# Performance work log

Hardware: AMD Instinct MI355X
Metric: run time of the kernel (lower is better)

Reference implementation:

```python
import jax, jax.numpy as jnp
import numpy as np

B, N, M, DQ, DK, DV, H = 8, 1024, 1024, 512, 512, 512, 8
DH = DV // H           # per-head dim (dim_split)
DFF = 4 * DV           # FFN hidden dim
EPS = 1e-5


def _layernorm(x, g, b):
    mu = jnp.mean(x, axis=-1, keepdims=True)
    var = jnp.mean(jnp.square(x - mu), axis=-1, keepdims=True)
    return (x - mu) * jax.lax.rsqrt(var + EPS) * g + b


def setup_inputs() -> dict:
    key = jax.random.key(0)
    ks = jax.random.split(key, 20)
    s = 0.02
    return {
        "Q": jax.random.normal(ks[0], (B, N, DQ), jnp.float32),
        "K": jax.random.normal(ks[1], (B, M, DK), jnp.float32),
        "Wq": jax.random.normal(ks[2], (DV, DQ), jnp.float32) * s,
        "bq": jnp.zeros((DV,), jnp.float32),
        "Wk": jax.random.normal(ks[3], (DV, DK), jnp.float32) * s,
        "bk": jnp.zeros((DV,), jnp.float32),
        "Wv": jax.random.normal(ks[4], (DV, DK), jnp.float32) * s,
        "bv": jnp.zeros((DV,), jnp.float32),
        "W1": jax.random.normal(ks[5], (DFF, DV), jnp.float32) * s,
        "b1": jnp.zeros((DFF,), jnp.float32),
        "W2": jax.random.normal(ks[6], (DFF, DFF), jnp.float32) * s,
        "b2": jnp.zeros((DFF,), jnp.float32),
        "W3": jax.random.normal(ks[7], (DV, DFF), jnp.float32) * s,
        "b3": jnp.zeros((DV,), jnp.float32),
        "g0": jnp.ones((DV,), jnp.float32),
        "beta0": jnp.zeros((DV,), jnp.float32),
        "g1": jnp.ones((DV,), jnp.float32),
        "beta1": jnp.zeros((DV,), jnp.float32),
    }


def reference(Q, K, Wq, bq, Wk, bk, Wv, bv, W1, b1, W2, b2, W3, b3, g0, beta0, g1, beta1):
    # projections (torch Linear: x @ W.T + b)
    Qp = Q @ Wq.T + bq            # [B, N, DV]
    Kp = K @ Wk.T + bk            # [B, M, DV]
    Vp = K @ Wv.T + bv            # [B, M, DV]

    # split heads: [B, S, DV] -> [B, S, H, DH]
    Qh = Qp.reshape(B, N, H, DH)
    Kh = Kp.reshape(B, M, H, DH)
    Vh = Vp.reshape(B, M, H, DH)

    # scaled dot-product attention (scale = sqrt(head_dim))
    A = jnp.einsum("bnhd,bmhd->bhnm", Qh, Kh) / jnp.sqrt(jnp.float32(DH))
    A = jax.nn.softmax(A, axis=-1)
    O = jnp.einsum("bhnm,bmhd->bnhd", A, Vh).reshape(B, N, DV)

    # residual with projected Q, then LN
    O = _layernorm(O + Qp, g0, beta0)

    # FFN: Linear->ReLU->Linear->ReLU->Linear (num_hidden_layers=2)
    h = jax.nn.relu(O @ W1.T + b1)
    h = jax.nn.relu(h @ W2.T + b2)
    Off = h @ W3.T + b3

    return _layernorm(O + Off, g1, beta1)
```

## Files before the change

### kernel.cpp

```cpp
#include <hip/hip_runtime.h>


typedef __bf16 bf16_t;
typedef __bf16 bf16x8 __attribute__((ext_vector_type(8)));
typedef __bf16 bf16x4 __attribute__((ext_vector_type(4)));
typedef __bf16 bf16x2 __attribute__((ext_vector_type(2)));
typedef float  f32x4  __attribute__((ext_vector_type(4)));
typedef float  f32x16 __attribute__((ext_vector_type(16)));
typedef int    i32x4_t __attribute__((ext_vector_type(4)));
typedef int    i32x8_t __attribute__((ext_vector_type(8)));

__device__ __forceinline__ f32x4 mfma16(bf16x8 a, bf16x8 b, f32x4 c) {
  return __builtin_amdgcn_mfma_f32_16x16x32_bf16(a, b, c, 0, 0, 0);
}

__device__ __forceinline__ void gload_lds16(const void* g, void* l) {
  __builtin_amdgcn_global_load_lds((const __attribute__((address_space(1))) void*)g,
                                   (__attribute__((address_space(3))) void*)l,
                                   16, 0, 0);
}

__device__ __forceinline__ unsigned char to_fp8(float v) {
  return (unsigned char)(__builtin_amdgcn_cvt_pk_fp8_f32(v, v, 0, false) & 0xff);
}

__global__ __launch_bounds__(256) void cast_all(
    const float* __restrict__ Q, const float* __restrict__ K,
    const float* __restrict__ Wq, const float* __restrict__ Wk,
    const float* __restrict__ Wv, const float* __restrict__ W1,
    const float* __restrict__ W2, const float* __restrict__ W3,
    bf16_t* Qb, bf16_t* Kb, bf16_t* Wqb, bf16_t* Wkb, bf16_t* Wvb,
    bf16_t* W1b, unsigned char* W2q, bf16_t* W3b)
{
  long i = ((long)blockIdx.x * 256 + threadIdx.x) * 4;
  if (i >= 10223616L && i < 14417920L) {
    long o = i - 10223616L;
    float4 v = *(const float4*)(W2 + o);
    unsigned int lo = __builtin_amdgcn_cvt_pk_fp8_f32(v.x, v.y, 0, false);
    unsigned int hi = __builtin_amdgcn_cvt_pk_fp8_f32(v.z, v.w, 0, false);
    *(unsigned int*)(W2q + o) = (lo & 0xffffu) | (hi << 16);
    return;
  }
  const float* s; bf16_t* d; long o;
  if      (i <  4194304L) { s = Q;  d = Qb;  o = i;             }
  else if (i <  8388608L) { s = K;  d = Kb;  o = i - 4194304L;  }
  else if (i <  8650752L) { s = Wq; d = Wqb; o = i - 8388608L;  }
  else if (i <  8912896L) { s = Wk; d = Wkb; o = i - 8650752L;  }
  else if (i <  9175040L) { s = Wv; d = Wvb; o = i - 8912896L;  }
  else if (i < 10223616L) { s = W1; d = W1b; o = i - 9175040L;  }
  else                    { s = W3; d = W3b; o = i - 14417920L; }
  float4 v = *(const float4*)(s + o);
  bf16x4 w;
  w[0] = (bf16_t)v.x; w[1] = (bf16_t)v.y; w[2] = (bf16_t)v.z; w[3] = (bf16_t)v.w;
  *(bf16x4*)(d + o) = w;
}

template <int BM, bool RELU, bool VTEPI, bool DBUF>
__device__ __forceinline__ void gemm_core(
    const bf16_t* __restrict__ A, const bf16_t* __restrict__ W,
    const float* __restrict__ bias, float* __restrict__ Cf,
    bf16_t* __restrict__ Cb, unsigned char* __restrict__ C8,
    bf16_t* __restrict__ VTout,
    float bscale, int N, int K, int lda, int ldb, int bx, int by)
{
  static_assert(BM == 128, "gemm_core tuned for BM=128");
  constexpr int FI = 4;
  constexpr int FJ = 4;
  constexpr int CN = 64;
  constexpr int AISS = 4;
  constexpr int SM_AB = (BM + 128) * 64 * 2;
  constexpr int SM_TS = 128 * 132 * 2;
  constexpr int SM_ONE = (VTEPI && SM_TS > SM_AB) ? SM_TS : SM_AB;
  constexpr int SMEM = DBUF ? 2 * SM_AB : SM_ONE;

  __shared__ __align__(16) char smem[SMEM];

  const int tid  = threadIdx.x;
  const int wave = tid >> 6, lane = tid & 63;
  const int lq   = lane & 15, quad = lane >> 4;
  const int wm   = wave & 1;
  const int wn   = wave >> 1;
  const long row0 = (long)bx * BM;
  const long col0 = (long)by * 128;

  const int sr = tid >> 3;
  const int cg = (tid & 7) ^ (sr & 7);
  const bf16_t* ag = A + (row0 + sr) * (long)lda + cg * 8;
  const bf16_t* bg = W + (col0 + sr) * (long)ldb + cg * 8;
  const int asOff = wave * 1024;
  const int bsOff = BM * 128 + wave * 1024;
  const long arows32 = 32L * lda;
  const long brows32 = 32L * ldb;

  auto stage = [&](int k0, int bi) {
    char* base = smem + (DBUF ? bi * SM_AB : 0);
#pragma unroll
    for (int is = 0; is < AISS; is++)
      gload_lds16(ag + is * arows32 + k0, base + asOff + is * 4096);
#pragma unroll
    for (int is = 0; is < 4; is++)
      gload_lds16(bg + is * brows32 + k0, base + bsOff + is * 4096);
  };

  const int off0 = (quad ^ (lq & 7)) * 8;
  const int aO0 = ((wm * 64 + lq) * 64 + off0) * 2;
  const int aO1 = ((wm * 64 + lq) * 64 + (off0 ^ 32)) * 2;
  const int bO0 = BM * 128 + ((wn * CN + lq) * 64 + off0) * 2;
  const int bO1 = BM * 128 + ((wn * CN + lq) * 64 + (off0 ^ 32)) * 2;

  f32x4 acc[FI][FJ];
#pragma unroll
  for (int i = 0; i < FI; i++)
#pragma unroll
    for (int j = 0; j < FJ; j++) acc[i][j] = (f32x4){0.f, 0.f, 0.f, 0.f};

  const int nt = K >> 6;
  if constexpr (DBUF) stage(0, 0);
  for (int t = 0; t < nt; ++t) {
    const char* base;
    if constexpr (DBUF) {
      const int cur = t & 1;
      if (t < nt - 1) {
        stage((t + 1) * 64, cur ^ 1);
        asm volatile("s_waitcnt vmcnt(8)" ::: "memory");
      } else {
        asm volatile("s_waitcnt vmcnt(0)" ::: "memory");
      }
      __builtin_amdgcn_s_barrier();
      __builtin_amdgcn_sched_barrier(0);
      base = smem + cur * SM_AB;
    } else {
      __syncthreads();
      stage(t * 64, 0);
      __syncthreads();
      base = smem;
    }

    bf16x8 af[FI], bw[FJ];
#pragma unroll
    for (int i = 0; i < FI; i++) af[i] = *(const bf16x8*)(base + aO0 + i * 2048);
#pragma unroll
    for (int j = 0; j < FJ; j++) bw[j] = *(const bf16x8*)(base + bO0 + j * 2048);
#pragma unroll
    for (int i = 0; i < FI; i++)
#pragma unroll
      for (int j = 0; j < FJ; j++)
        acc[i][j] = mfma16(af[i], bw[j], acc[i][j]);
#pragma unroll
    for (int i = 0; i < FI; i++) af[i] = *(const bf16x8*)(base + aO1 + i * 2048);
#pragma unroll
    for (int j = 0; j < FJ; j++) bw[j] = *(const bf16x8*)(base + bO1 + j * 2048);
#pragma unroll
    for (int i = 0; i < FI; i++)
#pragma unroll
      for (int j = 0; j < FJ; j++)
        acc[i][j] = mfma16(af[i], bw[j], acc[i][j]);

    if constexpr (DBUF) {
      __builtin_amdgcn_sched_barrier(0);
      __builtin_amdgcn_s_barrier();
    }
  }

  float bc[FJ];
#pragma unroll
  for (int j = 0; j < FJ; j++)
    bc[j] = bias ? bias[col0 + wn * CN + j * 16 + lq] : 0.f;

  if (VTEPI && VTout) {
    bf16_t* Ts = (bf16_t*)smem;
    __syncthreads();
#pragma unroll
    for (int i = 0; i < FI; i++)
#pragma unroll
      for (int j = 0; j < FJ; j++) {
        bf16x4 pv;
#pragma unroll
        for (int r = 0; r < 4; r++) pv[r] = (bf16_t)(acc[i][j][r] + bc[j]);
        *(bf16x4*)(Ts + (wn * CN + j * 16 + lq) * 132 + wm * 64 + i * 16 + quad * 4) = pv;
      }
    __syncthreads();
    const int b  = bx >> 3;
    const int mb = (bx & 7) * 128;
    const int h0 = by * 2;
    const int dd = tid >> 4;
    const int mc = (tid & 15) * 8;
#pragma unroll
    for (int p = 0; p < 8; p++) {
      const int d = dd + p * 16;
      bf16x8 v = *(const bf16x8*)(Ts + d * 132 + mc);
      *(bf16x8*)(VTout + ((long)(b * 8 + h0 + (d >> 6))) * 65536
                 + (d & 63) * 1024 + mb + mc) = v;
    }
    return;
  }

  const long rb = row0 + wm * 64 + quad * 4;
  const long cb = col0 + wn * CN + lq;
#pragma unroll
  for (int i = 0; i < FI; i++)
#pragma unroll
    for (int j = 0; j < FJ; j++)
#pragma unroll
      for (int r = 0; r < 4; r++) {
        float v = acc[i][j][r] + bc[j];
        if (RELU) v = fmaxf(v, 0.f);
        long idx = (rb + i * 16 + r) * (long)N + cb + j * 16;
        if (Cf) Cf[idx] = v;
        if (Cb) Cb[idx] = (bf16_t)(v * bscale);
        if (C8) C8[idx] = to_fp8(v);
      }
}

template <int BM, bool RELU>
__global__ __launch_bounds__(256) void gemm_bt(
    const bf16_t* __restrict__ A, const bf16_t* __restrict__ W,
    const float* __restrict__ bias, float* __restrict__ Cf,
    bf16_t* __restrict__ Cb, unsigned char* __restrict__ C8,
    float bscale, int N, int K)
{
  const int d  = blockIdx.x;
  const int bx = (d & 7) * 8 + ((d >> 3) & 7);
  const int by = d >> 6;
  gemm_core<BM, RELU, false, true>(A, W, bias, Cf, Cb, C8, nullptr, bscale,
                                   N, K, K, K, bx, by);
}

__global__ __launch_bounds__(256) void ffn3_splitk(
    const bf16_t* __restrict__ H2, const bf16_t* __restrict__ W3b,
    bf16_t* __restrict__ Off01)
{
  const int z = blockIdx.z;
  gemm_core<128, false, false, false>(H2 + z * 1024, W3b + z * 1024, nullptr,
                               nullptr, Off01 + (long)z * 4194304, nullptr,
                               nullptr, 1.0f, 512, 1024, 2048, 2048,
                               blockIdx.x, blockIdx.y);
}

__global__ __launch_bounds__(256) void proj3(
    const bf16_t* __restrict__ Qb, const bf16_t* __restrict__ Kb,
    const bf16_t* __restrict__ Wqb, const bf16_t* __restrict__ Wkb,
    const bf16_t* __restrict__ Wvb,
    const float* __restrict__ bq, const float* __restrict__ bk,
    const float* __restrict__ bv,
    bf16_t* Qpb, bf16_t* Kpb, bf16_t* VT)
{
  const int z = blockIdx.z;
  const bf16_t* A  = (z == 0) ? Qb : Kb;
  const bf16_t* Wt = (z == 0) ? Wqb : ((z == 1) ? Wkb : Wvb);
  const float* bias = (z == 0) ? bq : ((z == 1) ? bk : bv);
  bf16_t* Cb = (z == 0) ? Qpb : ((z == 1) ? Kpb : nullptr);
  bf16_t* VTout = (z == 2) ? VT : nullptr;
  const float sc = (z == 1) ? 0.125f : 1.0f;
  gemm_core<128, false, true, false>(A, Wt, bias, nullptr, Cb, nullptr, VTout, sc,
                              512, 512, 512, 512, blockIdx.x, blockIdx.y);
}

__global__ __launch_bounds__(256) void ffn2_fp8(
    const unsigned char* __restrict__ H1, const unsigned char* __restrict__ W2,
    const float* __restrict__ bias, bf16_t* __restrict__ C)
{
  __shared__ unsigned char As[16384];
  __shared__ unsigned char Bs[16384];
  const int tid = threadIdx.x;
  const int wave = tid >> 6, lane = tid & 63;
  const int wm = wave & 1, wn = wave >> 1;
  const int m = lane & 31, h = lane >> 5;
  const int d  = blockIdx.x;
  const int bxi = (d & 7) * 8 + ((d >> 3) & 7);
  const int byi = d >> 6;
  const long row0 = (long)bxi * 128;
  const long col0 = (long)byi * 128;

  const int sr = tid >> 3;
  const int cg = (tid & 7) ^ (sr & 7);
  const unsigned char* ag = H1 + (row0 + sr) * 2048 + cg * 16;
  const unsigned char* bg = W2 + (col0 + sr) * 2048 + cg * 16;
  char* asD = (char*)As + wave * 1024;
  char* bsD = (char*)Bs + wave * 1024;

  const int ar0 = wm * 64 + m, ar1 = ar0 + 32;
  const int br0 = wn * 64 + m, br1 = wn * 64 + 32 + m;

  f32x16 acc[2][2];
#pragma unroll
  for (int mi = 0; mi < 2; mi++)
#pragma unroll
    for (int nj = 0; nj < 2; nj++)
#pragma unroll
      for (int r = 0; r < 16; r++) acc[mi][nj][r] = 0.f;

  for (int k0 = 0; k0 < 2048; k0 += 128) {
    __syncthreads();
#pragma unroll
    for (int is = 0; is < 4; is++)
      gload_lds16(ag + is * 65536 + k0, asD + is * 4096);
#pragma unroll
    for (int is = 0; is < 4; is++)
      gload_lds16(bg + is * 65536 + k0, bsD + is * 4096);
    __syncthreads();
#pragma unroll
    for (int ks = 0; ks < 2; ks++) {
      const int c0 = ks * 4 + h * 2;
      i32x8_t a[2], b[2];
#pragma unroll
      for (int mi = 0; mi < 2; mi++) {
        const int r = mi ? ar1 : ar0;
        i32x4_t lo = *(const i32x4_t*)(As + r * 128 + ((c0    ) ^ (r & 7)) * 16);
        i32x4_t hi = *(const i32x4_t*)(As + r * 128 + ((c0 + 1) ^ (r & 7)) * 16);
        a[mi][0] = lo[0]; a[mi][1] = lo[1]; a[mi][2] = lo[2]; a[mi][3] = lo[3];
        a[mi][4] = hi[0]; a[mi][5] = hi[1]; a[mi][6] = hi[2]; a[mi][7] = hi[3];
      }
#pragma unroll
      for (int nj = 0; nj < 2; nj++) {
        const int r = nj ? br1 : br0;
        i32x4_t lo = *(const i32x4_t*)(Bs + r * 128 + ((c0    ) ^ (r & 7)) * 16);
        i32x4_t hi = *(const i32x4_t*)(Bs + r * 128 + ((c0 + 1) ^ (r & 7)) * 16);
        b[nj][0] = lo[0]; b[nj][1] = lo[1]; b[nj][2] = lo[2]; b[nj][3] = lo[3];
        b[nj][4] = hi[0]; b[nj][5] = hi[1]; b[nj][6] = hi[2]; b[nj][7] = hi[3];
      }
#pragma unroll
      for (int mi = 0; mi < 2; mi++)
#pragma unroll
        for (int nj = 0; nj < 2; nj++)
          acc[mi][nj] = __builtin_amdgcn_mfma_scale_f32_32x32x64_f8f6f4(
              a[mi], b[nj], acc[mi][nj], 0, 0,
              0, 0x7f7f7f7f, 0, 0x7f7f7f7f);
    }
  }

  float bc[2];
  bc[0] = bias[col0 + wn * 64 + m];
  bc[1] = bias[col0 + wn * 64 + 32 + m];
#pragma unroll
  for (int mi = 0; mi < 2; mi++)
#pragma unroll
    for (int nj = 0; nj < 2; nj++)
#pragma unroll
      for (int reg = 0; reg < 16; reg++) {
        const int rl = (reg & 3) + 8 * (reg >> 2) + 4 * h;
        float v = fmaxf(acc[mi][nj][reg] + bc[nj], 0.f);
        C[(row0 + wm * 64 + mi * 32 + rl) * 2048 + col0 + wn * 64 + nj * 32 + m]
            = (bf16_t)v;
      }
}

__global__ __launch_bounds__(256) void attn(
    const bf16_t* __restrict__ Qp, const bf16_t* __restrict__ Kp,
    const bf16_t* __restrict__ VT, bf16_t* __restrict__ O)
{
  const int d0 = blockIdx.x;
  const int j  = d0 >> 3;
  const int g  = (d0 & 7) * 8 + (j >> 3);
  const int qb = j & 7;
  const int h  = g & 7, b = g >> 3;

  const int tid = threadIdx.x;
  const int wave = tid >> 6, lane = tid & 63;
  const int lq = lane & 15, quad = lane >> 4;

  __shared__ bf16_t Ks[2][8192];
  __shared__ bf16_t VTs[2][8192];
  __shared__ bf16_t Ps[4][16 * 72];

  const long bh = (long)b * 1024;
  const int qrowA = qb * 128 + wave * 16 + lq;
  const int qrowB = qrowA + 64;

  const bf16_t* qpA = Qp + (bh + qrowA) * 512 + h * 64 + quad * 8;
  const bf16_t* qpB = Qp + (bh + qrowB) * 512 + h * 64 + quad * 8;
  const bf16x8 qfA0 = *(const bf16x8*)qpA;
  const bf16x8 qfA1 = *(const bf16x8*)(qpA + 32);
  const bf16x8 qfB0 = *(const bf16x8*)qpB;
  const bf16x8 qfB1 = *(const bf16x8*)(qpB + 32);

  f32x4 oaccA[4], oaccB[4];
#pragma unroll
  for (int t = 0; t < 4; t++) {
    oaccA[t] = (f32x4){0.f, 0.f, 0.f, 0.f};
    oaccB[t] = (f32x4){0.f, 0.f, 0.f, 0.f};
  }
  float lA = 0.f, lB = 0.f;

  const int sr = tid >> 3;
  const int cg = (tid & 7) ^ (sr & 7);
  const bf16_t* kg  = Kp + bh * 512 + h * 64;
  const bf16_t* vtg = VT + ((long)b * 8 + h) * 65536;
  const int off0 = (quad ^ (lq & 7)) * 8;

  auto stage = [&](int m0, int bi) {
    char* ksDst = (char*)(Ks[bi]) + wave * 1024;
    char* vtDst = (char*)(VTs[bi]) + wave * 1024;
#pragma unroll
    for (int s = 0; s < 2; s++) {
      gload_lds16(kg + (long)(m0 + s * 64 + sr) * 512 + cg * 8,      ksDst + s * 8192);
      gload_lds16(kg + (long)(m0 + s * 64 + sr + 32) * 512 + cg * 8, ksDst + s * 8192 + 4096);
      gload_lds16(vtg + (long)sr * 1024 + m0 + s * 64 + cg * 8,        vtDst + s * 8192);
      gload_lds16(vtg + (long)(sr + 32) * 1024 + m0 + s * 64 + cg * 8, vtDst + s * 8192 + 4096);
    }
  };

  stage(0, 0);

  for (int t = 0; t < 8; ++t) {
    const int cur = t & 1;
    if (t < 7) {
      stage((t + 1) * 128, cur ^ 1);
      asm volatile("s_waitcnt vmcnt(8)" ::: "memory");
    } else {
      asm volatile("s_waitcnt vmcnt(0)" ::: "memory");
    }
    __builtin_amdgcn_s_barrier();
    __builtin_amdgcn_sched_barrier(0);

    const bf16_t* Kc = Ks[cur];
    const bf16_t* Vc = VTs[cur];

    f32x4 stA[8], stB[8];
#pragma unroll
    for (int tt = 0; tt < 8; tt++) {
      const bf16_t* kb = Kc + (tt >> 2) * 4096 + ((tt & 3) * 16 + lq) * 64;
      bf16x8 ka0 = *(const bf16x8*)(kb + off0);
      bf16x8 ka1 = *(const bf16x8*)(kb + (off0 ^ 32));
      f32x4 sA = (f32x4){0.f, 0.f, 0.f, 0.f};
      sA = mfma16(ka0, qfA0, sA);
      sA = mfma16(ka1, qfA1, sA);
      stA[tt] = sA;
      f32x4 sB = (f32x4){0.f, 0.f, 0.f, 0.f};
      sB = mfma16(ka0, qfB0, sB);
      sB = mfma16(ka1, qfB1, sB);
      stB[tt] = sB;
    }

    float lsA = 0.f, lsB = 0.f;
#pragma unroll
    for (int tt = 0; tt < 8; tt++)
#pragma unroll
      for (int r = 0; r < 4; r++) {
        float pA = __expf(stA[tt][r]);
        stA[tt][r] = pA;
        lsA += pA;
        float pB = __expf(stB[tt][r]);
        stB[tt][r] = pB;
        lsB += pB;
      }
    lsA += __shfl_xor(lsA, 16, 64);
    lsA += __shfl_xor(lsA, 32, 64);
    lA += lsA;
    lsB += __shfl_xor(lsB, 16, 64);
    lsB += __shfl_xor(lsB, 32, 64);
    lB += lsB;

    bf16_t* pw = &Ps[wave][0];
#pragma unroll
    for (int hh = 0; hh < 2; hh++) {
#pragma unroll
      for (int tt = 0; tt < 4; tt++) {
        bf16x4 pv;
#pragma unroll
        for (int r = 0; r < 4; r++) pv[r] = (bf16_t)stA[hh * 4 + tt][r];
        *(bf16x4*)(pw + lq * 72 + tt * 16 + quad * 4) = pv;
      }
#pragma unroll
      for (int ks = 0; ks < 2; ks++) {
        bf16x8 pb = *(const bf16x8*)(pw + lq * 72 + ks * 32 + quad * 8);
#pragma unroll
        for (int dt = 0; dt < 4; dt++) {
          const bf16_t* vb = Vc + hh * 4096 + (dt * 16 + lq) * 64;
          bf16x8 va = *(const bf16x8*)(vb + (ks ? (off0 ^ 32) : off0));
          oaccA[dt] = mfma16(va, pb, oaccA[dt]);
        }
      }
    }
#pragma unroll
    for (int hh = 0; hh < 2; hh++) {
#pragma unroll
      for (int tt = 0; tt < 4; tt++) {
        bf16x4 pv;
#pragma unroll
        for (int r = 0; r < 4; r++) pv[r] = (bf16_t)stB[hh * 4 + tt][r];
        *(bf16x4*)(pw + lq * 72 + tt * 16 + quad * 4) = pv;
      }
#pragma unroll
      for (int ks = 0; ks < 2; ks++) {
        bf16x8 pb = *(const bf16x8*)(pw + lq * 72 + ks * 32 + quad * 8);
#pragma unroll
        for (int dt = 0; dt < 4; dt++) {
          const bf16_t* vb = Vc + hh * 4096 + (dt * 16 + lq) * 64;
          bf16x8 va = *(const bf16x8*)(vb + (ks ? (off0 ^ 32) : off0));
          oaccB[dt] = mfma16(va, pb, oaccB[dt]);
        }
      }
    }

    __builtin_amdgcn_sched_barrier(0);
    __builtin_amdgcn_s_barrier();
  }

  const float invA = 1.f / lA;
  const float invB = 1.f / lB;
  bf16_t* opA = O + (bh + qrowA) * 512 + h * 64 + quad * 4;
  bf16_t* opB = O + (bh + qrowB) * 512 + h * 64 + quad * 4;
#pragma unroll
  for (int dt = 0; dt < 4; dt++) {
    bf16x4 vA, vB;
#pragma unroll
    for (int r = 0; r < 4; r++) {
      vA[r] = (bf16_t)(oaccA[dt][r] * invA);
      vB[r] = (bf16_t)(oaccB[dt][r] * invB);
    }
    *(bf16x4*)(opA + dt * 16) = vA;
    *(bf16x4*)(opB + dt * 16) = vB;
  }
}

__device__ __forceinline__ float2 ld2(const float* p, long row, int tid) {
  return ((const float2*)(p + row * 512))[tid];
}
__device__ __forceinline__ float2 ld2(const bf16_t* p, long row, int tid) {
  bf16x2 v = *(const bf16x2*)(p + row * 512 + tid * 2);
  return make_float2((float)v[0], (float)v[1]);
}

__device__ __forceinline__ void ln_finish(
    float x0, float x1, const float* g, const float* be, int tid,
    int wave, int lane, float* of, bf16_t* ob, long row)
{
  float s = x0 + x1, ss = x0 * x0 + x1 * x1;
#pragma unroll
  for (int off = 1; off < 64; off <<= 1) {
    s  += __shfl_xor(s,  off, 64);
    ss += __shfl_xor(ss, off, 64);
  }
  __shared__ float sm[8];
  if (lane == 0) { sm[wave] = s; sm[4 + wave] = ss; }
  __syncthreads();
  s  = sm[0] + sm[1] + sm[2] + sm[3];
  ss = sm[4] + sm[5] + sm[6] + sm[7];
  const float mu = s * (1.f / 512.f);
  const float var = ss * (1.f / 512.f) - mu * mu;
  const float rs = rsqrtf(var + 1e-5f);
  const float2 gg = ((const float2*)g)[tid];
  const float2 bb = ((const float2*)be)[tid];
  const float o0 = (x0 - mu) * rs * gg.x + bb.x;
  const float o1 = (x1 - mu) * rs * gg.y + bb.y;
  if (of) ((float2*)(of + row * 512))[tid] = make_float2(o0, o1);
  if (ob) {
    bf16x2 t; t[0] = (bf16_t)o0; t[1] = (bf16_t)o1;
    *(bf16x2*)(ob + row * 512 + tid * 2) = t;
  }
}

__global__ __launch_bounds__(256) void ln_res(
    const bf16_t* __restrict__ A, const bf16_t* __restrict__ Bv,
    const float* __restrict__ g, const float* __restrict__ be,
    bf16_t* __restrict__ ob)
{
  const int row = blockIdx.x, tid = threadIdx.x;
  const float2 va = ld2(A,  (long)row, tid);
  const float2 vb = ld2(Bv, (long)row, tid);
  ln_finish(va.x + vb.x, va.y + vb.y, g, be, tid, tid >> 6, tid & 63,
            nullptr, ob, row);
}

__global__ __launch_bounds__(256) void ln_res3(
    const bf16_t* __restrict__ X, const bf16_t* __restrict__ O0,
    const bf16_t* __restrict__ O1, const float* __restrict__ bias,
    const float* __restrict__ g, const float* __restrict__ be,
    float* __restrict__ of)
{
  const int row = blockIdx.x, tid = threadIdx.x;
  const float2 vx = ld2(X,  (long)row, tid);
  const float2 v0 = ld2(O0, (long)row, tid);
  const float2 v1 = ld2(O1, (long)row, tid);
  const float2 vb = ((const float2*)bias)[tid];
  ln_finish(vx.x + v0.x + v1.x + vb.x, vx.y + v0.y + v1.y + vb.y,
            g, be, tid, tid >> 6, tid & 63, of, nullptr, row);
}

extern "C" void kernel_launch(void* const* d_in, const int* in_sizes, int n_in,
                              void* d_out, int out_size, void* d_ws, size_t ws_size,
                              hipStream_t stream)
{
  const float* Q   = (const float*)d_in[0];
  const float* K   = (const float*)d_in[1];
  const float* Wq  = (const float*)d_in[2];
  const float* bq  = (const float*)d_in[3];
  const float* Wk  = (const float*)d_in[4];
  const float* bk  = (const float*)d_in[5];
  const float* Wv  = (const float*)d_in[6];
  const float* bv  = (const float*)d_in[7];
  const float* W1  = (const float*)d_in[8];
  const float* b1  = (const float*)d_in[9];
  const float* W2  = (const float*)d_in[10];
  const float* b2  = (const float*)d_in[11];
  const float* W3  = (const float*)d_in[12];
  const float* b3  = (const float*)d_in[13];
  const float* g0  = (const float*)d_in[14];
  const float* be0 = (const float*)d_in[15];
  const float* g1  = (const float*)d_in[16];
  const float* be1 = (const float*)d_in[17];

  char* ws = (char*)d_ws;
  bf16_t* Wqb = (bf16_t*)(ws + 0);
  bf16_t* Wkb = (bf16_t*)(ws + 524288);
  bf16_t* Wvb = (bf16_t*)(ws + 1048576);
  bf16_t* W1b = (bf16_t*)(ws + 1572864);
  bf16_t* W3b = (bf16_t*)(ws + 3670016);
  unsigned char* W2q = (unsigned char*)(ws + 5767168);
  bf16_t* Qb  = (bf16_t*)(ws + 14155776);
  bf16_t* Kb  = (bf16_t*)(ws + 22544384);
  bf16_t* Qpb = (bf16_t*)(ws + 30932992);
  bf16_t* Kpb = (bf16_t*)(ws + 39321600);
  bf16_t* VT  = (bf16_t*)(ws + 47710208);
  bf16_t* Of  = (bf16_t*)(ws + 14155776);
  bf16_t* Xb  = (bf16_t*)(ws + 22544384);
  bf16_t* H2  = (bf16_t*)(ws + 30932992);
  unsigned char* H1q = (unsigned char*)(ws + 64487424);
  bf16_t* Off0 = (bf16_t*)(ws + 64487424);
  bf16_t* Off1 = (bf16_t*)(ws + 72876032);
  float*  out = (float*)d_out;

  cast_all<<<15104, 256, 0, stream>>>(Q, K, Wq, Wk, Wv, W1, W2, W3,
                                      Qb, Kb, Wqb, Wkb, Wvb, W1b, W2q, W3b);
  proj3<<<dim3(64, 4, 3), 256, 0, stream>>>(Qb, Kb, Wqb, Wkb, Wvb, bq, bk, bv,
                                            Qpb, Kpb, VT);
  attn<<<dim3(512, 1, 1), 256, 0, stream>>>(Qpb, Kpb, VT, Of);
  ln_res<<<8192, 256, 0, stream>>>(Of, Qpb, g0, be0, Xb);
  gemm_bt<128, true ><<<dim3(1024, 1, 1), 256, 0, stream>>>(Xb, W1b, b1, nullptr, nullptr, H1q, 1.0f, 2048, 512);
  ffn2_fp8<<<dim3(1024, 1, 1), 256, 0, stream>>>(H1q, W2q, b2, H2);
  ffn3_splitk<<<dim3(64, 4, 2), 256, 0, stream>>>(H2, W3b, Off0);
  ln_res3<<<8192, 256, 0, stream>>>(Xb, Off0, Off1, b3, g1, be1, out);
}
```

Measured before the change: 274.6 us.

## Move all FFN GEMMs to FP8 with a shared fp8 GEMM core

Quantizes W1 and W3 to FP8 alongside W2, has the first layernorm also emit an FP8 copy of its output, and runs FFN1, FFN2 and FFN3 through one templated FP8 MFMA GEMM core. FFN2 now writes FP8 activations instead of bf16, and FFN3 becomes an FP8 split-K GEMM. The goal is to halve operand bytes and use the faster FP8 MFMA path for the FFN. The cost is lower precision, which adds more error. The bf16 GEMM path drops double buffering since only proj3 still uses it, and the FFN launches lose the swizzled block ordering.

```diff
diff --git a/kernel.cpp b/kernel.cpp
--- a/kernel.cpp
+++ b/kernel.cpp
@@ -30,15 +30,18 @@
     const float* __restrict__ Wv, const float* __restrict__ W1,
     const float* __restrict__ W2, const float* __restrict__ W3,
     bf16_t* Qb, bf16_t* Kb, bf16_t* Wqb, bf16_t* Wkb, bf16_t* Wvb,
-    bf16_t* W1b, unsigned char* W2q, bf16_t* W3b)
+    unsigned char* W1q, unsigned char* W2q, unsigned char* W3q)
 {
   long i = ((long)blockIdx.x * 256 + threadIdx.x) * 4;
-  if (i >= 10223616L && i < 14417920L) {
-    long o = i - 10223616L;
-    float4 v = *(const float4*)(W2 + o);
+  if (i >= 9175040L) {
+    const float* s; unsigned char* d; long o;
+    if      (i < 10223616L) { s = W1; d = W1q; o = i - 9175040L;  }
+    else if (i < 14417920L) { s = W2; d = W2q; o = i - 10223616L; }
+    else                    { s = W3; d = W3q; o = i - 14417920L; }
+    float4 v = *(const float4*)(s + o);
     unsigned int lo = __builtin_amdgcn_cvt_pk_fp8_f32(v.x, v.y, 0, false);
     unsigned int hi = __builtin_amdgcn_cvt_pk_fp8_f32(v.z, v.w, 0, false);
-    *(unsigned int*)(W2q + o) = (lo & 0xffffu) | (hi << 16);
+    *(unsigned int*)(d + o) = (lo & 0xffffu) | (hi << 16);
     return;
   }
   const float* s; bf16_t* d; long o;
@@ -46,32 +49,26 @@
   else if (i <  8388608L) { s = K;  d = Kb;  o = i - 4194304L;  }
   else if (i <  8650752L) { s = Wq; d = Wqb; o = i - 8388608L;  }
   else if (i <  8912896L) { s = Wk; d = Wkb; o = i - 8650752L;  }
-  else if (i <  9175040L) { s = Wv; d = Wvb; o = i - 8912896L;  }
-  else if (i < 10223616L) { s = W1; d = W1b; o = i - 9175040L;  }
-  else                    { s = W3; d = W3b; o = i - 14417920L; }
+  else                    { s = Wv; d = Wvb; o = i - 8912896L;  }
   float4 v = *(const float4*)(s + o);
   bf16x4 w;
   w[0] = (bf16_t)v.x; w[1] = (bf16_t)v.y; w[2] = (bf16_t)v.z; w[3] = (bf16_t)v.w;
   *(bf16x4*)(d + o) = w;
 }
 
-template <int BM, bool RELU, bool VTEPI, bool DBUF>
+template <bool VTEPI>
 __device__ __forceinline__ void gemm_core(
     const bf16_t* __restrict__ A, const bf16_t* __restrict__ W,
-    const float* __restrict__ bias, float* __restrict__ Cf,
-    bf16_t* __restrict__ Cb, unsigned char* __restrict__ C8,
-    bf16_t* __restrict__ VTout,
+    const float* __restrict__ bias,
+    bf16_t* __restrict__ Cb, bf16_t* __restrict__ VTout,
     float bscale, int N, int K, int lda, int ldb, int bx, int by)
 {
-  static_assert(BM == 128, "gemm_core tuned for BM=128");
   constexpr int FI = 4;
   constexpr int FJ = 4;
   constexpr int CN = 64;
-  constexpr int AISS = 4;
-  constexpr int SM_AB = (BM + 128) * 64 * 2;
+  constexpr int SM_AB = 256 * 64 * 2;
   constexpr int SM_TS = 128 * 132 * 2;
-  constexpr int SM_ONE = (VTEPI && SM_TS > SM_AB) ? SM_TS : SM_AB;
-  constexpr int SMEM = DBUF ? 2 * SM_AB : SM_ONE;
+  constexpr int SMEM = (VTEPI && SM_TS > SM_AB) ? SM_TS : SM_AB;
 
   __shared__ __align__(16) char smem[SMEM];
 
@@ -80,7 +77,7 @@
   const int lq   = lane & 15, quad = lane >> 4;
   const int wm   = wave & 1;
   const int wn   = wave >> 1;
-  const long row0 = (long)bx * BM;
+  const long row0 = (long)bx * 128;
   const long col0 = (long)by * 128;
 
   const int sr = tid >> 3;
@@ -88,25 +85,24 @@
   const bf16_t* ag = A + (row0 + sr) * (long)lda + cg * 8;
   const bf16_t* bg = W + (col0 + sr) * (long)ldb + cg * 8;
   const int asOff = wave * 1024;
-  const int bsOff = BM * 128 + wave * 1024;
+  const int bsOff = 128 * 128 + wave * 1024;
   const long arows32 = 32L * lda;
   const long brows32 = 32L * ldb;
 
-  auto stage = [&](int k0, int bi) {
-    char* base = smem + (DBUF ? bi * SM_AB : 0);
-#pragma unroll
-    for (int is = 0; is < AISS; is++)
-      gload_lds16(ag + is * arows32 + k0, base + asOff + is * 4096);
+  auto stage = [&](int k0) {
 #pragma unroll
     for (int is = 0; is < 4; is++)
-      gload_lds16(bg + is * brows32 + k0, base + bsOff + is * 4096);
+      gload_lds16(ag + is * arows32 + k0, smem + asOff + is * 4096);
+#pragma unroll
+    for (int is = 0; is < 4; is++)
+      gload_lds16(bg + is * brows32 + k0, smem + bsOff + is * 4096);
   };
 
   const int off0 = (quad ^ (lq & 7)) * 8;
   const int aO0 = ((wm * 64 + lq) * 64 + off0) * 2;
   const int aO1 = ((wm * 64 + lq) * 64 + (off0 ^ 32)) * 2;
-  const int bO0 = BM * 128 + ((wn * CN + lq) * 64 + off0) * 2;
-  const int bO1 = BM * 128 + ((wn * CN + lq) * 64 + (off0 ^ 32)) * 2;
+  const int bO0 = 128 * 128 + ((wn * CN + lq) * 64 + off0) * 2;
+  const int bO1 = 128 * 128 + ((wn * CN + lq) * 64 + (off0 ^ 32)) * 2;
 
   f32x4 acc[FI][FJ];
 #pragma unroll
@@ -115,51 +111,30 @@
     for (int j = 0; j < FJ; j++) acc[i][j] = (f32x4){0.f, 0.f, 0.f, 0.f};
 
   const int nt = K >> 6;
-  if constexpr (DBUF) stage(0, 0);
   for (int t = 0; t < nt; ++t) {
-    const char* base;
-    if constexpr (DBUF) {
-      const int cur = t & 1;
-      if (t < nt - 1) {
-        stage((t + 1) * 64, cur ^ 1);
-        asm volatile("s_waitcnt vmcnt(8)" ::: "memory");
-      } else {
-        asm volatile("s_waitcnt vmcnt(0)" ::: "memory");
-      }
-      __builtin_amdgcn_s_barrier();
-      __builtin_amdgcn_sched_barrier(0);
-      base = smem + cur * SM_AB;
-    } else {
-      __syncthreads();
-      stage(t * 64, 0);
-      __syncthreads();
-      base = smem;
-    }
+    __syncthreads();
+    stage(t * 64);
+    __syncthreads();
 
     bf16x8 af[FI], bw[FJ];
 #pragma unroll
-    for (int i = 0; i < FI; i++) af[i] = *(const bf16x8*)(base + aO0 + i * 2048);
-#pragma unroll
-    for (int j = 0; j < FJ; j++) bw[j] = *(const bf16x8*)(base + bO0 + j * 2048);
+    for (int i = 0; i < FI; i++) af[i] = *(const bf16x8*)(smem + aO0 + i * 2048);
+#pragma unroll
+    for (int j = 0; j < FJ; j++) bw[j] = *(const bf16x8*)(smem + bO0 + j * 2048);
 #pragma unroll
     for (int i = 0; i < FI; i++)
 #pragma unroll
       for (int j = 0; j < FJ; j++)
         acc[i][j] = mfma16(af[i], bw[j], acc[i][j]);
 #pragma unroll
-    for (int i = 0; i < FI; i++) af[i] = *(const bf16x8*)(base + aO1 + i * 2048);
-#pragma unroll
-    for (int j = 0; j < FJ; j++) bw[j] = *(const bf16x8*)(base + bO1 + j * 2048);
+    for (int i = 0; i < FI; i++) af[i] = *(const bf16x8*)(smem + aO1 + i * 2048);
+#pragma unroll
+    for (int j = 0; j < FJ; j++) bw[j] = *(const bf16x8*)(smem + bO1 + j * 2048);
 #pragma unroll
     for (int i = 0; i < FI; i++)
 #pragma unroll
       for (int j = 0; j < FJ; j++)
         acc[i][j] = mfma16(af[i], bw[j], acc[i][j]);
-
-    if constexpr (DBUF) {
-      __builtin_amdgcn_sched_barrier(0);
-      __builtin_amdgcn_s_barrier();
-    }
   }
 
   float bc[FJ];
@@ -204,37 +179,9 @@
 #pragma unroll
       for (int r = 0; r < 4; r++) {
         float v = acc[i][j][r] + bc[j];
-        if (RELU) v = fmaxf(v, 0.f);
         long idx = (rb + i * 16 + r) * (long)N + cb + j * 16;
-        if (Cf) Cf[idx] = v;
         if (Cb) Cb[idx] = (bf16_t)(v * bscale);
-        if (C8) C8[idx] = to_fp8(v);
-      }
-}
-
-template <int BM, bool RELU>
-__global__ __launch_bounds__(256) void gemm_bt(
-    const bf16_t* __restrict__ A, const bf16_t* __restrict__ W,
-    const float* __restrict__ bias, float* __restrict__ Cf,
-    bf16_t* __restrict__ Cb, unsigned char* __restrict__ C8,
-    float bscale, int N, int K)
-{
-  const int d  = blockIdx.x;
-  const int bx = (d & 7) * 8 + ((d >> 3) & 7);
-  const int by = d >> 6;
-  gemm_core<BM, RELU, false, true>(A, W, bias, Cf, Cb, C8, nullptr, bscale,
-                                   N, K, K, K, bx, by);
-}
-
-__global__ __launch_bounds__(256) void ffn3_splitk(
-    const bf16_t* __restrict__ H2, const bf16_t* __restrict__ W3b,
-    bf16_t* __restrict__ Off01)
-{
-  const int z = blockIdx.z;
-  gemm_core<128, false, false, false>(H2 + z * 1024, W3b + z * 1024, nullptr,
-                               nullptr, Off01 + (long)z * 4194304, nullptr,
-                               nullptr, 1.0f, 512, 1024, 2048, 2048,
-                               blockIdx.x, blockIdx.y);
+      }
 }
 
 __global__ __launch_bounds__(256) void proj3(
@@ -252,13 +199,16 @@
   bf16_t* Cb = (z == 0) ? Qpb : ((z == 1) ? Kpb : nullptr);
   bf16_t* VTout = (z == 2) ? VT : nullptr;
   const float sc = (z == 1) ? 0.125f : 1.0f;
-  gemm_core<128, false, true, false>(A, Wt, bias, nullptr, Cb, nullptr, VTout, sc,
-                              512, 512, 512, 512, blockIdx.x, blockIdx.y);
-}
-
-__global__ __launch_bounds__(256) void ffn2_fp8(
-    const unsigned char* __restrict__ H1, const unsigned char* __restrict__ W2,
-    const float* __restrict__ bias, bf16_t* __restrict__ C)
+  gemm_core<true>(A, Wt, bias, Cb, VTout, sc,
+                  512, 512, 512, 512, blockIdx.x, blockIdx.y);
+}
+
+template <int OUT>
+__device__ __forceinline__ void fp8_gemm_core(
+    const unsigned char* __restrict__ A, const unsigned char* __restrict__ B,
+    const float* __restrict__ bias, unsigned char* __restrict__ C8,
+    bf16_t* __restrict__ Cb, int ldab, int K, int koff, int N,
+    int bxi, int byi)
 {
   __shared__ unsigned char As[16384];
   __shared__ unsigned char Bs[16384];
@@ -266,18 +216,16 @@
   const int wave = tid >> 6, lane = tid & 63;
   const int wm = wave & 1, wn = wave >> 1;
   const int m = lane & 31, h = lane >> 5;
-  const int d  = blockIdx.x;
-  const int bxi = (d & 7) * 8 + ((d >> 3) & 7);
-  const int byi = d >> 6;
   const long row0 = (long)bxi * 128;
   const long col0 = (long)byi * 128;
 
   const int sr = tid >> 3;
   const int cg = (tid & 7) ^ (sr & 7);
-  const unsigned char* ag = H1 + (row0 + sr) * 2048 + cg * 16;
-  const unsigned char* bg = W2 + (col0 + sr) * 2048 + cg * 16;
+  const unsigned char* ag = A + (row0 + sr) * (long)ldab + koff + cg * 16;
+  const unsigned char* bg = B + (col0 + sr) * (long)ldab + koff + cg * 16;
   char* asD = (char*)As + wave * 1024;
   char* bsD = (char*)Bs + wave * 1024;
+  const long rows32 = 32L * ldab;
 
   const int ar0 = wm * 64 + m, ar1 = ar0 + 32;
   const int br0 = wn * 64 + m, br1 = wn * 64 + 32 + m;
@@ -290,14 +238,14 @@
 #pragma unroll
       for (int r = 0; r < 16; r++) acc[mi][nj][r] = 0.f;
 
-  for (int k0 = 0; k0 < 2048; k0 += 128) {
+  for (int k0 = 0; k0 < K; k0 += 128) {
     __syncthreads();
 #pragma unroll
     for (int is = 0; is < 4; is++)
-      gload_lds16(ag + is * 65536 + k0, asD + is * 4096);
+      gload_lds16(ag + is * rows32 + k0, asD + is * 4096);
 #pragma unroll
     for (int is = 0; is < 4; is++)
-      gload_lds16(bg + is * 65536 + k0, bsD + is * 4096);
+      gload_lds16(bg + is * rows32 + k0, bsD + is * 4096);
     __syncthreads();
 #pragma unroll
     for (int ks = 0; ks < 2; ks++) {
@@ -330,8 +278,8 @@
   }
 
   float bc[2];
-  bc[0] = bias[col0 + wn * 64 + m];
-  bc[1] = bias[col0 + wn * 64 + 32 + m];
+  bc[0] = bias ? bias[col0 + wn * 64 + m] : 0.f;
+  bc[1] = bias ? bias[col0 + wn * 64 + 32 + m] : 0.f;
 #pragma unroll
   for (int mi = 0; mi < 2; mi++)
 #pragma unroll
@@ -339,10 +287,40 @@
 #pragma unroll
       for (int reg = 0; reg < 16; reg++) {
         const int rl = (reg & 3) + 8 * (reg >> 2) + 4 * h;
-        float v = fmaxf(acc[mi][nj][reg] + bc[nj], 0.f);
-        C[(row0 + wm * 64 + mi * 32 + rl) * 2048 + col0 + wn * 64 + nj * 32 + m]
-            = (bf16_t)v;
-      }
+        const long idx = (row0 + wm * 64 + mi * 32 + rl) * (long)N
+                       + col0 + wn * 64 + nj * 32 + m;
+        if (OUT == 0) {
+          float v = fmaxf(acc[mi][nj][reg] + bc[nj], 0.f);
+          C8[idx] = to_fp8(v);
+        } else {
+          Cb[idx] = (bf16_t)acc[mi][nj][reg];
+        }
+      }
+}
+
+__global__ __launch_bounds__(256) void ffn1_fp8(
+    const unsigned char* __restrict__ Xq, const unsigned char* __restrict__ W1,
+    const float* __restrict__ bias, unsigned char* __restrict__ C)
+{
+  fp8_gemm_core<0>(Xq, W1, bias, C, nullptr, 512, 512, 0, 2048,
+                   blockIdx.x, blockIdx.y);
+}
+
+__global__ __launch_bounds__(256) void ffn2_fp8(
+    const unsigned char* __restrict__ H1, const unsigned char* __restrict__ W2,
+    const float* __restrict__ bias, unsigned char* __restrict__ C)
+{
+  fp8_gemm_core<0>(H1, W2, bias, C, nullptr, 2048, 2048, 0, 2048,
+                   blockIdx.x, blockIdx.y);
+}
+
+__global__ __launch_bounds__(256) void ffn3_fp8(
+    const unsigned char* __restrict__ H2, const unsigned char* __restrict__ W3,
+    bf16_t* __restrict__ Off01)
+{
+  const int z = blockIdx.z;
+  fp8_gemm_core<1>(H2, W3, nullptr, nullptr, Off01 + (long)z * 4194304,
+                   2048, 1024, z * 1024, 512, blockIdx.x, blockIdx.y);
 }
 
 __global__ __launch_bounds__(256) void attn(
@@ -524,7 +502,7 @@
 
 __device__ __forceinline__ void ln_finish(
     float x0, float x1, const float* g, const float* be, int tid,
-    int wave, int lane, float* of, bf16_t* ob, long row)
+    int wave, int lane, float* of, bf16_t* ob, unsigned char* o8, long row)
 {
   float s = x0 + x1, ss = x0 * x0 + x1 * x1;
 #pragma unroll
@@ -549,18 +527,22 @@
     bf16x2 t; t[0] = (bf16_t)o0; t[1] = (bf16_t)o1;
     *(bf16x2*)(ob + row * 512 + tid * 2) = t;
   }
+  if (o8) {
+    unsigned int p = __builtin_amdgcn_cvt_pk_fp8_f32(o0, o1, 0, false);
+    *(unsigned short*)(o8 + row * 512 + tid * 2) = (unsigned short)(p & 0xffffu);
+  }
 }
 
 __global__ __launch_bounds__(256) void ln_res(
     const bf16_t* __restrict__ A, const bf16_t* __restrict__ Bv,
     const float* __restrict__ g, const float* __restrict__ be,
-    bf16_t* __restrict__ ob)
+    bf16_t* __restrict__ ob, unsigned char* __restrict__ o8)
 {
   const int row = blockIdx.x, tid = threadIdx.x;
   const float2 va = ld2(A,  (long)row, tid);
   const float2 vb = ld2(Bv, (long)row, tid);
   ln_finish(va.x + vb.x, va.y + vb.y, g, be, tid, tid >> 6, tid & 63,
-            nullptr, ob, row);
+            nullptr, ob, o8, row);
 }
 
 __global__ __launch_bounds__(256) void ln_res3(
@@ -575,7 +557,7 @@
   const float2 v1 = ld2(O1, (long)row, tid);
   const float2 vb = ((const float2*)bias)[tid];
   ln_finish(vx.x + v0.x + v1.x + vb.x, vx.y + v0.y + v1.y + vb.y,
-            g, be, tid, tid >> 6, tid & 63, of, nullptr, row);
+            g, be, tid, tid >> 6, tid & 63, of, nullptr, nullptr, row);
 }
 
 extern "C" void kernel_launch(void* const* d_in, const int* in_sizes, int n_in,
@@ -605,8 +587,8 @@
   bf16_t* Wqb = (bf16_t*)(ws + 0);
   bf16_t* Wkb = (bf16_t*)(ws + 524288);
   bf16_t* Wvb = (bf16_t*)(ws + 1048576);
-  bf16_t* W1b = (bf16_t*)(ws + 1572864);
-  bf16_t* W3b = (bf16_t*)(ws + 3670016);
+  unsigned char* W1q = (unsigned char*)(ws + 1572864);
+  unsigned char* W3q = (unsigned char*)(ws + 3670016);
   unsigned char* W2q = (unsigned char*)(ws + 5767168);
   bf16_t* Qb  = (bf16_t*)(ws + 14155776);
   bf16_t* Kb  = (bf16_t*)(ws + 22544384);
@@ -615,20 +597,21 @@
   bf16_t* VT  = (bf16_t*)(ws + 47710208);
   bf16_t* Of  = (bf16_t*)(ws + 14155776);
   bf16_t* Xb  = (bf16_t*)(ws + 22544384);
-  bf16_t* H2  = (bf16_t*)(ws + 30932992);
+  unsigned char* Xq = (unsigned char*)(ws + 47710208);
+  unsigned char* H2q = (unsigned char*)(ws + 30932992);
   unsigned char* H1q = (unsigned char*)(ws + 64487424);
   bf16_t* Off0 = (bf16_t*)(ws + 64487424);
   bf16_t* Off1 = (bf16_t*)(ws + 72876032);
   float*  out = (float*)d_out;
 
   cast_all<<<15104, 256, 0, stream>>>(Q, K, Wq, Wk, Wv, W1, W2, W3,
-                                      Qb, Kb, Wqb, Wkb, Wvb, W1b, W2q, W3b);
+                                      Qb, Kb, Wqb, Wkb, Wvb, W1q, W2q, W3q);
   proj3<<<dim3(64, 4, 3), 256, 0, stream>>>(Qb, Kb, Wqb, Wkb, Wvb, bq, bk, bv,
                                             Qpb, Kpb, VT);
   attn<<<dim3(512, 1, 1), 256, 0, stream>>>(Qpb, Kpb, VT, Of);
-  ln_res<<<8192, 256, 0, stream>>>(Of, Qpb, g0, be0, Xb);
-  gemm_bt<128, true ><<<dim3(1024, 1, 1), 256, 0, stream>>>(Xb, W1b, b1, nullptr, nullptr, H1q, 1.0f, 2048, 512);
-  ffn2_fp8<<<dim3(1024, 1, 1), 256, 0, stream>>>(H1q, W2q, b2, H2);
-  ffn3_splitk<<<dim3(64, 4, 2), 256, 0, stream>>>(H2, W3b, Off0);
+  ln_res<<<8192, 256, 0, stream>>>(Of, Qpb, g0, be0, Xb, Xq);
+  ffn1_fp8<<<dim3(64, 16), 256, 0, stream>>>(Xq, W1q, b1, H1q);
+  ffn2_fp8<<<dim3(64, 16), 256, 0, stream>>>(H1q, W2q, b2, H2q);
+  ffn3_fp8<<<dim3(64, 4, 2), 256, 0, stream>>>(H2q, W3q, Off0);
   ln_res3<<<8192, 256, 0, stream>>>(Xb, Off0, Off1, b3, g1, be1, out);
 }
```

After: 252.6 us. 1.09x faster.
